# Optimization experiments

Hardware: AMD Instinct MI355X
Metric: run time of the kernel (lower is better)

Reference implementation:

```python
import jax, jax.numpy as jnp
import numpy as np

SCALE = 8.0  # sqrt(head_dim=64)

def setup_inputs() -> dict:
    key = jax.random.key(0)
    kq, kk, kv = jax.random.split(key, 3)
    B, H, S, D = 2, 16, 2048, 64
    return {
        "query": jax.random.normal(kq, (B, H, S, D), dtype=jnp.float32),
        "key": jax.random.normal(kk, (B, H, S, D), dtype=jnp.float32),
        "value": jax.random.normal(kv, (B, H, S, D), dtype=jnp.float32),
        "mask": jnp.ones((B, 1, 1, S), dtype=jnp.int32),
    }

def reference(query, key, value, mask):
    # scores: [B,H,S,S]
    scores = jnp.einsum("bhqd,bhkd->bhqk", query, key) / SCALE
    scores = jnp.where(mask == 0, -jnp.inf, scores)
    attn_probs = jax.nn.softmax(scores, axis=-1)
    # dropout_rate = 0.0 -> identity
    output = jnp.einsum("bhqk,bhkd->bhqd", attn_probs, value)
    return (output, attn_probs)
```

## Files before the change

kernel.cpp:

```cpp
#include <hip/hip_runtime.h>

#define B_  2
#define H_  16
#define S_  2048
#define D_  64
#define BH_ (B_*H_)
#define QT  64
#define KT  64
#define NKT (S_/KT)
#define LDQ 72

typedef __attribute__((ext_vector_type(8))) short bf16x8;
typedef __attribute__((ext_vector_type(4))) float f32x4;

static __device__ __forceinline__ ushort f2bf(float f) {
  union { float f; unsigned u; } v; v.f = f;
  unsigned r = (v.u + 0x7fff + ((v.u >> 16) & 1)) >> 16;
  return (ushort)r;
}

static __device__ __forceinline__ void score_tiles(
    f32x4 acc[4], const ushort* __restrict__ sK, const bf16x8 qa[2],
    int l15, int lq, const int* __restrict__ mg, int kbase)
{
#pragma unroll
  for (int t = 0; t < 4; ++t) {
    const bf16x8 kb0 = *(const bf16x8*)&sK[(t*16 + l15)*LDQ +      lq*8];
    const bf16x8 kb1 = *(const bf16x8*)&sK[(t*16 + l15)*LDQ + 32 + lq*8];
    f32x4 a = {0.f, 0.f, 0.f, 0.f};
    a = __builtin_amdgcn_mfma_f32_16x16x32_bf16(qa[0], kb0, a, 0, 0, 0);
    a = __builtin_amdgcn_mfma_f32_16x16x32_bf16(qa[1], kb1, a, 0, 0, 0);
    const int mv = mg[kbase + t*16 + l15];
    if (mv == 0) { a[0] = -1e30f; a[1] = -1e30f; a[2] = -1e30f; a[3] = -1e30f; }
    acc[t] = a;
  }
}

__global__ __launch_bounds__(256)
void attn_kernel(const float* __restrict__ Q, const float* __restrict__ K,
                 const float* __restrict__ V, const int* __restrict__ mask,
                 float* __restrict__ outO, float* __restrict__ outP)
{
  __shared__ ushort sQ[QT * LDQ];
  __shared__ ushort sK[KT * LDQ];
  __shared__ ushort sVt[D_ * LDQ];
  __shared__ ushort sP[4][16 * LDQ];

  const int tid  = threadIdx.x;
  const int wave = tid >> 6;
  const int lane = tid & 63;
  const int l15  = lane & 15;
  const int lq   = lane >> 4;

  const int qt = blockIdx.x;
  const int bh = blockIdx.y;
  const int b  = bh >> 4;
  const int q0 = qt * QT;

  const float* Qg = Q + (size_t)(bh*S_ + q0) * D_;
  const float* Kg = K + (size_t)bh * S_ * D_;
  const float* Vg = V + (size_t)bh * S_ * D_;
  const int*   mg = mask + b * S_;
  float* Og = outO + (size_t)(bh*S_ + q0) * D_;
  float* Pg = outP + ((size_t)(bh*S_ + q0)) * S_;

  const int srow = tid >> 2;
  const int sd0  = (tid & 3) * 16;

  {
    const float* src = Qg + (size_t)srow * D_ + sd0;
    ushort* dst = &sQ[srow*LDQ + sd0];
#pragma unroll
    for (int i = 0; i < 16; i += 4) {
      float4 v = *(const float4*)(src + i);
      dst[i+0] = f2bf(v.x * 0.125f);
      dst[i+1] = f2bf(v.y * 0.125f);
      dst[i+2] = f2bf(v.z * 0.125f);
      dst[i+3] = f2bf(v.w * 0.125f);
    }
  }
  __syncthreads();

  bf16x8 qa[2];
#pragma unroll
  for (int c = 0; c < 2; ++c)
    qa[c] = *(const bf16x8*)&sQ[(wave*16 + l15)*LDQ + c*32 + lq*8];

  float m_r[4] = {-1e30f, -1e30f, -1e30f, -1e30f};
  float l_r[4] = {0.f, 0.f, 0.f, 0.f};

  for (int kt = 0; kt < NKT; ++kt) {
    __syncthreads();
    {
      const float* src = Kg + (size_t)(kt*KT + srow) * D_ + sd0;
      ushort* dst = &sK[srow*LDQ + sd0];
#pragma unroll
      for (int i = 0; i < 16; i += 4) {
        float4 v = *(const float4*)(src + i);
        dst[i+0] = f2bf(v.x); dst[i+1] = f2bf(v.y);
        dst[i+2] = f2bf(v.z); dst[i+3] = f2bf(v.w);
      }
    }
    __syncthreads();

    f32x4 acc[4];
    score_tiles(acc, sK, qa, l15, lq, mg, kt*KT);

#pragma unroll
    for (int j = 0; j < 4; ++j) {
      float v = fmaxf(fmaxf(acc[0][j], acc[1][j]), fmaxf(acc[2][j], acc[3][j]));
#pragma unroll
      for (int s = 1; s < 16; s <<= 1) v = fmaxf(v, __shfl_xor(v, s));
      const float mn = fmaxf(m_r[j], v);
      float ps = __expf(acc[0][j] - mn) + __expf(acc[1][j] - mn)
               + __expf(acc[2][j] - mn) + __expf(acc[3][j] - mn);
#pragma unroll
      for (int s = 1; s < 16; s <<= 1) ps += __shfl_xor(ps, s);
      l_r[j] = l_r[j] * __expf(m_r[j] - mn) + ps;
      m_r[j] = mn;
    }
  }

  float inv_l[4];
#pragma unroll
  for (int j = 0; j < 4; ++j) inv_l[j] = 1.0f / l_r[j];

  f32x4 oacc[4];
#pragma unroll
  for (int n = 0; n < 4; ++n) { oacc[n][0]=0.f; oacc[n][1]=0.f; oacc[n][2]=0.f; oacc[n][3]=0.f; }

  ushort* sPw = &sP[wave][0];

  for (int kt = 0; kt < NKT; ++kt) {
    __syncthreads();
    {
      const float* src = Kg + (size_t)(kt*KT + srow) * D_ + sd0;
      ushort* dst = &sK[srow*LDQ + sd0];
#pragma unroll
      for (int i = 0; i < 16; i += 4) {
        float4 v = *(const float4*)(src + i);
        dst[i+0] = f2bf(v.x); dst[i+1] = f2bf(v.y);
        dst[i+2] = f2bf(v.z); dst[i+3] = f2bf(v.w);
      }
    }
    {
      const int vkey = tid & 63;
      const int vd0  = (tid >> 6) * 16;
      const float* vsrc = Vg + (size_t)(kt*KT + vkey) * D_ + vd0;
#pragma unroll
      for (int i = 0; i < 16; i += 4) {
        float4 v = *(const float4*)(vsrc + i);
        sVt[(vd0+i+0)*LDQ + vkey] = f2bf(v.x);
        sVt[(vd0+i+1)*LDQ + vkey] = f2bf(v.y);
        sVt[(vd0+i+2)*LDQ + vkey] = f2bf(v.z);
        sVt[(vd0+i+3)*LDQ + vkey] = f2bf(v.w);
      }
    }
    __syncthreads();

    f32x4 acc[4];
    score_tiles(acc, sK, qa, l15, lq, mg, kt*KT);

#pragma unroll
    for (int t = 0; t < 4; ++t) {
#pragma unroll
      for (int j = 0; j < 4; ++j) {
        const float p = __expf(acc[t][j] - m_r[j]) * inv_l[j];
        sPw[(lq*4 + j)*LDQ + t*16 + l15] = f2bf(p);
      }
    }
    __syncthreads();

#pragma unroll
    for (int i = 0; i < 4; ++i) {
      const int r = lq + i*4;
      const ushort* ps = &sPw[r*LDQ + l15*4];
      float4 o;
      o.x = __uint_as_float((unsigned)ps[0] << 16);
      o.y = __uint_as_float((unsigned)ps[1] << 16);
      o.z = __uint_as_float((unsigned)ps[2] << 16);
      o.w = __uint_as_float((unsigned)ps[3] << 16);
      *(float4*)&Pg[(size_t)(wave*16 + r)*S_ + kt*KT + l15*4] = o;
    }

#pragma unroll
    for (int c = 0; c < 2; ++c) {
      const bf16x8 pa = *(const bf16x8*)&sPw[l15*LDQ + c*32 + lq*8];
#pragma unroll
      for (int n = 0; n < 4; ++n) {
        const bf16x8 vb = *(const bf16x8*)&sVt[(n*16 + l15)*LDQ + c*32 + lq*8];
        oacc[n] = __builtin_amdgcn_mfma_f32_16x16x32_bf16(pa, vb, oacc[n], 0, 0, 0);
      }
    }
  }

#pragma unroll
  for (int n = 0; n < 4; ++n) {
#pragma unroll
    for (int j = 0; j < 4; ++j) {
      Og[(size_t)(wave*16 + lq*4 + j)*D_ + n*16 + l15] = oacc[n][j];
    }
  }
}

extern "C" void kernel_launch(void* const* d_in, const int* in_sizes, int n_in,
                              void* d_out, int out_size, void* d_ws, size_t ws_size,
                              hipStream_t stream) {
  const float* Q = (const float*)d_in[0];
  const float* K = (const float*)d_in[1];
  const float* V = (const float*)d_in[2];
  const int* mask = (const int*)d_in[3];
  float* outO = (float*)d_out;
  float* outP = outO + (size_t)B_ * H_ * S_ * D_;
  dim3 grid(S_ / QT, BH_);
  attn_kernel<<<grid, dim3(256), 0, stream>>>(Q, K, V, mask, outO, outP);
}
```

Before: 776.5 us.

## Pre-convert Q/K/V to swizzled bf16 tiles and double-buffer async LDS loads

Adds a conversion kernel that turns Q (scaled by log2e/8), K, and transposed V into bf16 64x64 tiles with an XOR swizzle, stored in the workspace. The main kernel then stages these tiles into double-buffered LDS with global_load_lds, prefetching the next tile while computing on the current one. The softmax switches to exp2 with a single logsumexp offset, and the cross-lane max/sum reduction moves out of the first pass to the end. This removes the repeated fp32 loads and conversions of K/V in every query block, at the cost of an extra launch and workspace traffic. The old kernel is kept as a fallback when the workspace is too small.

```diff
diff --git a/kernel.cpp b/kernel.cpp
--- a/kernel.cpp
+++ b/kernel.cpp
@@ -5,13 +5,16 @@
 #define S_  2048
 #define D_  64
 #define BH_ (B_*H_)
-#define QT  64
-#define KT  64
-#define NKT (S_/KT)
+#define NKT (S_/64)
 #define LDQ 72
+#define LDP 72
 
 typedef __attribute__((ext_vector_type(8))) short bf16x8;
 typedef __attribute__((ext_vector_type(4))) float f32x4;
+typedef __attribute__((address_space(1))) const char gchar;
+typedef __attribute__((address_space(3))) char lchar;
+
+#define QK_SCALE 0.18033688011112042f
 
 static __device__ __forceinline__ ushort f2bf(float f) {
   union { float f; unsigned u; } v; v.f = f;
@@ -19,7 +22,228 @@
   return (ushort)r;
 }
 
-static __device__ __forceinline__ void score_tiles(
+static __device__ __forceinline__ uint4 pack8(const float* e, float sc) {
+  uint4 p;
+  p.x = (unsigned)f2bf(e[0]*sc) | ((unsigned)f2bf(e[1]*sc) << 16);
+  p.y = (unsigned)f2bf(e[2]*sc) | ((unsigned)f2bf(e[3]*sc) << 16);
+  p.z = (unsigned)f2bf(e[4]*sc) | ((unsigned)f2bf(e[5]*sc) << 16);
+  p.w = (unsigned)f2bf(e[6]*sc) | ((unsigned)f2bf(e[7]*sc) << 16);
+  return p;
+}
+
+__global__ __launch_bounds__(256)
+void conv_kernel(const float* __restrict__ Q, const float* __restrict__ K,
+                 const float* __restrict__ V,
+                 ushort* __restrict__ Qw, ushort* __restrict__ Kw, ushort* __restrict__ Vw)
+{
+  const int tile = blockIdx.x, bh = blockIdx.y, mode = blockIdx.z;
+  const int tid = threadIdx.x;
+  const float* src = (mode == 0 ? Q : (mode == 1 ? K : V)) + ((size_t)bh*S_ + tile*64) * D_;
+  ushort* dst = (mode == 0 ? Qw : (mode == 1 ? Kw : Vw)) + ((size_t)bh*NKT + tile) * 4096;
+
+  const int r  = tid >> 2;
+  const int c0 = (tid & 3) * 16;
+
+  if (mode < 2) {
+    const float sc = (mode == 0) ? QK_SCALE : 1.0f;
+    const float4* s4 = (const float4*)(src + (size_t)r*D_ + c0);
+    float e[16];
+#pragma unroll
+    for (int i = 0; i < 4; ++i) {
+      float4 v = s4[i];
+      e[i*4+0] = v.x; e[i*4+1] = v.y; e[i*4+2] = v.z; e[i*4+3] = v.w;
+    }
+#pragma unroll
+    for (int g = 0; g < 2; ++g) {
+      const int gi = ((c0 >> 3) + g) ^ (r & 7);
+      *(uint4*)((char*)dst + r*128 + gi*16) = pack8(e + g*8, sc);
+    }
+  } else {
+    __shared__ float t[64][65];
+    const float4* s4 = (const float4*)(src + (size_t)r*D_ + c0);
+#pragma unroll
+    for (int i = 0; i < 4; ++i) {
+      float4 v = s4[i];
+      t[r][c0 + i*4 + 0] = v.x; t[r][c0 + i*4 + 1] = v.y;
+      t[r][c0 + i*4 + 2] = v.z; t[r][c0 + i*4 + 3] = v.w;
+    }
+    __syncthreads();
+    float e[16];
+#pragma unroll
+    for (int i = 0; i < 16; ++i) e[i] = t[c0 + i][r];
+#pragma unroll
+    for (int g = 0; g < 2; ++g) {
+      const int gi = ((c0 >> 3) + g) ^ (r & 7);
+      *(uint4*)((char*)dst + r*128 + gi*16) = pack8(e + g*8, 1.0f);
+    }
+  }
+}
+
+static __device__ __forceinline__ void stage8k(void* lds, const void* src, int wave, int lane) {
+  const char* s = (const char*)src + lane*16;
+  char* d = (char*)lds;
+#pragma unroll
+  for (int i = 0; i < 2; ++i) {
+    const int off = (wave + i*4) << 10;
+    __builtin_amdgcn_global_load_lds((gchar*)(s + off), (lchar*)(d + off), 16, 0, 0);
+  }
+}
+
+__global__ __launch_bounds__(256, 3)
+void attn2_kernel(const ushort* __restrict__ Qw, const ushort* __restrict__ Kw,
+                  const ushort* __restrict__ Vw, const int* __restrict__ mask,
+                  float* __restrict__ outO, float* __restrict__ outP)
+{
+  __shared__ ushort sQ[4096];
+  __shared__ ushort sK[2][4096];
+  __shared__ ushort sVt[2][4096];
+  __shared__ ushort sP[4][16 * LDP];
+
+  const int tid  = threadIdx.x;
+  const int wave = tid >> 6;
+  const int lane = tid & 63;
+  const int l15  = lane & 15;
+  const int lq   = lane >> 4;
+  const int rxor = l15 & 7;
+
+  const int qt = blockIdx.x;
+  const int bh = blockIdx.y;
+  const int b  = bh >> 4;
+
+  const ushort* Qt = Qw + ((size_t)bh*NKT + qt) * 4096;
+  const ushort* Kt = Kw + (size_t)bh*NKT * 4096;
+  const ushort* Vt = Vw + (size_t)bh*NKT * 4096;
+  const int*    mg = mask + b * S_;
+  float* Og = outO + (size_t)(bh*S_ + qt*64) * D_;
+  float* Pg = outP + (size_t)(bh*S_ + qt*64) * S_;
+
+  stage8k(sQ, Qt, wave, lane);
+  stage8k(sK[0], Kt, wave, lane);
+  __syncthreads();
+
+  bf16x8 qa[2];
+#pragma unroll
+  for (int c = 0; c < 2; ++c)
+    qa[c] = *(const bf16x8*)((const char*)sQ + (wave*16 + l15)*128 + (((c*4 + lq) ^ rxor) << 4));
+
+  float m_r[4] = {-1e30f, -1e30f, -1e30f, -1e30f};
+  float l_r[4] = {0.f, 0.f, 0.f, 0.f};
+
+  int cur = 0;
+  for (int kt = 0; kt < NKT; ++kt) {
+    if (kt + 1 < NKT) stage8k(sK[cur ^ 1], Kt + (size_t)(kt + 1)*4096, wave, lane);
+    int mv[4];
+#pragma unroll
+    for (int t = 0; t < 4; ++t) mv[t] = mg[kt*64 + t*16 + l15];
+    f32x4 acc[4];
+#pragma unroll
+    for (int t = 0; t < 4; ++t) {
+      const char* rowp = (const char*)sK[cur] + (t*16 + l15)*128;
+      const bf16x8 kb0 = *(const bf16x8*)(rowp + (((0 + lq) ^ rxor) << 4));
+      const bf16x8 kb1 = *(const bf16x8*)(rowp + (((4 + lq) ^ rxor) << 4));
+      f32x4 a = {0.f, 0.f, 0.f, 0.f};
+      a = __builtin_amdgcn_mfma_f32_16x16x32_bf16(qa[0], kb0, a, 0, 0, 0);
+      a = __builtin_amdgcn_mfma_f32_16x16x32_bf16(qa[1], kb1, a, 0, 0, 0);
+      if (mv[t] == 0) { a[0] = -1e30f; a[1] = -1e30f; a[2] = -1e30f; a[3] = -1e30f; }
+      acc[t] = a;
+    }
+#pragma unroll
+    for (int j = 0; j < 4; ++j) {
+      const float vmax = fmaxf(fmaxf(acc[0][j], acc[1][j]), fmaxf(acc[2][j], acc[3][j]));
+      const float mn = fmaxf(m_r[j], vmax);
+      const float ps = __builtin_amdgcn_exp2f(acc[0][j] - mn) + __builtin_amdgcn_exp2f(acc[1][j] - mn)
+                     + __builtin_amdgcn_exp2f(acc[2][j] - mn) + __builtin_amdgcn_exp2f(acc[3][j] - mn);
+      l_r[j] = l_r[j] * __builtin_amdgcn_exp2f(m_r[j] - mn) + ps;
+      m_r[j] = mn;
+    }
+    __syncthreads();
+    cur ^= 1;
+  }
+
+  float madj[4];
+#pragma unroll
+  for (int j = 0; j < 4; ++j) {
+    float m = m_r[j], l = l_r[j];
+#pragma unroll
+    for (int s = 1; s < 16; s <<= 1) {
+      const float om = __shfl_xor(m, s);
+      const float ol = __shfl_xor(l, s);
+      const float mn = fmaxf(m, om);
+      l = l * __builtin_amdgcn_exp2f(m - mn) + ol * __builtin_amdgcn_exp2f(om - mn);
+      m = mn;
+    }
+    madj[j] = m + __builtin_amdgcn_logf(l);
+  }
+
+  f32x4 oacc[4];
+#pragma unroll
+  for (int n = 0; n < 4; ++n) { oacc[n][0]=0.f; oacc[n][1]=0.f; oacc[n][2]=0.f; oacc[n][3]=0.f; }
+  ushort* sPw = &sP[wave][0];
+
+  stage8k(sK[0], Kt, wave, lane);
+  stage8k(sVt[0], Vt, wave, lane);
+  cur = 0;
+  __syncthreads();
+
+  for (int kt = 0; kt < NKT; ++kt) {
+    if (kt + 1 < NKT) {
+      stage8k(sK[cur ^ 1], Kt + (size_t)(kt + 1)*4096, wave, lane);
+      stage8k(sVt[cur ^ 1], Vt + (size_t)(kt + 1)*4096, wave, lane);
+    }
+    int mv[4];
+#pragma unroll
+    for (int t = 0; t < 4; ++t) mv[t] = mg[kt*64 + t*16 + l15];
+    f32x4 acc[4];
+#pragma unroll
+    for (int t = 0; t < 4; ++t) {
+      const char* rowp = (const char*)sK[cur] + (t*16 + l15)*128;
+      const bf16x8 kb0 = *(const bf16x8*)(rowp + (((0 + lq) ^ rxor) << 4));
+      const bf16x8 kb1 = *(const bf16x8*)(rowp + (((4 + lq) ^ rxor) << 4));
+      f32x4 a = {0.f, 0.f, 0.f, 0.f};
+      a = __builtin_amdgcn_mfma_f32_16x16x32_bf16(qa[0], kb0, a, 0, 0, 0);
+      a = __builtin_amdgcn_mfma_f32_16x16x32_bf16(qa[1], kb1, a, 0, 0, 0);
+      if (mv[t] == 0) { a[0] = -1e30f; a[1] = -1e30f; a[2] = -1e30f; a[3] = -1e30f; }
+      acc[t] = a;
+    }
+#pragma unroll
+    for (int t = 0; t < 4; ++t) {
+#pragma unroll
+      for (int j = 0; j < 4; ++j) {
+        sPw[(lq*4 + j)*LDP + t*16 + l15] = f2bf(__builtin_amdgcn_exp2f(acc[t][j] - madj[j]));
+      }
+    }
+#pragma unroll
+    for (int i = 0; i < 4; ++i) {
+      const int r = lq + i*4;
+      const ushort* ps = &sPw[r*LDP + l15*4];
+      float4 o;
+      o.x = __uint_as_float((unsigned)ps[0] << 16);
+      o.y = __uint_as_float((unsigned)ps[1] << 16);
+      o.z = __uint_as_float((unsigned)ps[2] << 16);
+      o.w = __uint_as_float((unsigned)ps[3] << 16);
+      *(float4*)&Pg[(size_t)(wave*16 + r)*S_ + kt*64 + l15*4] = o;
+    }
+#pragma unroll
+    for (int c2 = 0; c2 < 2; ++c2) {
+      const bf16x8 pa = *(const bf16x8*)((const char*)sPw + l15*(LDP*2) + c2*64 + lq*16);
+#pragma unroll
+      for (int n = 0; n < 4; ++n) {
+        const bf16x8 vb = *(const bf16x8*)((const char*)sVt[cur] + (n*16 + l15)*128 + (((c2*4 + lq) ^ rxor) << 4));
+        oacc[n] = __builtin_amdgcn_mfma_f32_16x16x32_bf16(pa, vb, oacc[n], 0, 0, 0);
+      }
+    }
+    __syncthreads();
+    cur ^= 1;
+  }
+
+#pragma unroll
+  for (int n = 0; n < 4; ++n)
+#pragma unroll
+    for (int j = 0; j < 4; ++j)
+      Og[(size_t)(wave*16 + lq*4 + j)*D_ + n*16 + l15] = oacc[n][j];
+}
+
+static __device__ __forceinline__ void score_tiles_fb(
     f32x4 acc[4], const ushort* __restrict__ sK, const bf16x8 qa[2],
     int l15, int lq, const int* __restrict__ mg, int kbase)
 {
@@ -41,8 +265,8 @@
                  const float* __restrict__ V, const int* __restrict__ mask,
                  float* __restrict__ outO, float* __restrict__ outP)
 {
-  __shared__ ushort sQ[QT * LDQ];
-  __shared__ ushort sK[KT * LDQ];
+  __shared__ ushort sQ[64 * LDQ];
+  __shared__ ushort sK[64 * LDQ];
   __shared__ ushort sVt[D_ * LDQ];
   __shared__ ushort sP[4][16 * LDQ];
 
@@ -51,11 +275,10 @@
   const int lane = tid & 63;
   const int l15  = lane & 15;
   const int lq   = lane >> 4;
-
   const int qt = blockIdx.x;
   const int bh = blockIdx.y;
   const int b  = bh >> 4;
-  const int q0 = qt * QT;
+  const int q0 = qt * 64;
 
   const float* Qg = Q + (size_t)(bh*S_ + q0) * D_;
   const float* Kg = K + (size_t)bh * S_ * D_;
@@ -73,10 +296,8 @@
 #pragma unroll
     for (int i = 0; i < 16; i += 4) {
       float4 v = *(const float4*)(src + i);
-      dst[i+0] = f2bf(v.x * 0.125f);
-      dst[i+1] = f2bf(v.y * 0.125f);
-      dst[i+2] = f2bf(v.z * 0.125f);
-      dst[i+3] = f2bf(v.w * 0.125f);
+      dst[i+0] = f2bf(v.x * 0.125f); dst[i+1] = f2bf(v.y * 0.125f);
+      dst[i+2] = f2bf(v.z * 0.125f); dst[i+3] = f2bf(v.w * 0.125f);
     }
   }
   __syncthreads();
@@ -92,7 +313,7 @@
   for (int kt = 0; kt < NKT; ++kt) {
     __syncthreads();
     {
-      const float* src = Kg + (size_t)(kt*KT + srow) * D_ + sd0;
+      const float* src = Kg + (size_t)(kt*64 + srow) * D_ + sd0;
       ushort* dst = &sK[srow*LDQ + sd0];
 #pragma unroll
       for (int i = 0; i < 16; i += 4) {
@@ -102,10 +323,8 @@
       }
     }
     __syncthreads();
-
     f32x4 acc[4];
-    score_tiles(acc, sK, qa, l15, lq, mg, kt*KT);
-
+    score_tiles_fb(acc, sK, qa, l15, lq, mg, kt*64);
 #pragma unroll
     for (int j = 0; j < 4; ++j) {
       float v = fmaxf(fmaxf(acc[0][j], acc[1][j]), fmaxf(acc[2][j], acc[3][j]));
@@ -128,13 +347,12 @@
   f32x4 oacc[4];
 #pragma unroll
   for (int n = 0; n < 4; ++n) { oacc[n][0]=0.f; oacc[n][1]=0.f; oacc[n][2]=0.f; oacc[n][3]=0.f; }
-
   ushort* sPw = &sP[wave][0];
 
   for (int kt = 0; kt < NKT; ++kt) {
     __syncthreads();
     {
-      const float* src = Kg + (size_t)(kt*KT + srow) * D_ + sd0;
+      const float* src = Kg + (size_t)(kt*64 + srow) * D_ + sd0;
       ushort* dst = &sK[srow*LDQ + sd0];
 #pragma unroll
       for (int i = 0; i < 16; i += 4) {
@@ -146,7 +364,7 @@
     {
       const int vkey = tid & 63;
       const int vd0  = (tid >> 6) * 16;
-      const float* vsrc = Vg + (size_t)(kt*KT + vkey) * D_ + vd0;
+      const float* vsrc = Vg + (size_t)(kt*64 + vkey) * D_ + vd0;
 #pragma unroll
       for (int i = 0; i < 16; i += 4) {
         float4 v = *(const float4*)(vsrc + i);
@@ -157,20 +375,16 @@
       }
     }
     __syncthreads();
-
     f32x4 acc[4];
-    score_tiles(acc, sK, qa, l15, lq, mg, kt*KT);
-
-#pragma unroll
-    for (int t = 0; t < 4; ++t) {
+    score_tiles_fb(acc, sK, qa, l15, lq, mg, kt*64);
+#pragma unroll
+    for (int t = 0; t < 4; ++t)
 #pragma unroll
       for (int j = 0; j < 4; ++j) {
         const float p = __expf(acc[t][j] - m_r[j]) * inv_l[j];
         sPw[(lq*4 + j)*LDQ + t*16 + l15] = f2bf(p);
       }
-    }
-    __syncthreads();
-
+    __syncthreads();
 #pragma unroll
     for (int i = 0; i < 4; ++i) {
       const int r = lq + i*4;
@@ -180,9 +394,8 @@
       o.y = __uint_as_float((unsigned)ps[1] << 16);
       o.z = __uint_as_float((unsigned)ps[2] << 16);
       o.w = __uint_as_float((unsigned)ps[3] << 16);
-      *(float4*)&Pg[(size_t)(wave*16 + r)*S_ + kt*KT + l15*4] = o;
-    }
-
+      *(float4*)&Pg[(size_t)(wave*16 + r)*S_ + kt*64 + l15*4] = o;
+    }
 #pragma unroll
     for (int c = 0; c < 2; ++c) {
       const bf16x8 pa = *(const bf16x8*)&sPw[l15*LDQ + c*32 + lq*8];
@@ -193,14 +406,11 @@
       }
     }
   }
-
-#pragma unroll
-  for (int n = 0; n < 4; ++n) {
-#pragma unroll
-    for (int j = 0; j < 4; ++j) {
+#pragma unroll
+  for (int n = 0; n < 4; ++n)
+#pragma unroll
+    for (int j = 0; j < 4; ++j)
       Og[(size_t)(wave*16 + lq*4 + j)*D_ + n*16 + l15] = oacc[n][j];
-    }
-  }
 }
 
 extern "C" void kernel_launch(void* const* d_in, const int* in_sizes, int n_in,
@@ -212,6 +422,15 @@
   const int* mask = (const int*)d_in[3];
   float* outO = (float*)d_out;
   float* outP = outO + (size_t)B_ * H_ * S_ * D_;
-  dim3 grid(S_ / QT, BH_);
-  attn_kernel<<<grid, dim3(256), 0, stream>>>(Q, K, V, mask, outO, outP);
-}
+
+  const size_t elems = (size_t)B_ * H_ * S_ * D_;
+  if (ws_size >= elems * 2 * 3) {
+    ushort* Qw = (ushort*)d_ws;
+    ushort* Kw = Qw + elems;
+    ushort* Vw = Kw + elems;
+    conv_kernel<<<dim3(NKT, BH_, 3), dim3(256), 0, stream>>>(Q, K, V, Qw, Kw, Vw);
+    attn2_kernel<<<dim3(S_/64, BH_), dim3(256), 0, stream>>>(Qw, Kw, Vw, mask, outO, outP);
+  } else {
+    attn_kernel<<<dim3(S_/64, BH_), dim3(256), 0, stream>>>(Q, K, V, mask, outO, outP);
+  }
+}
```

After: 707.2 us. -8.9%, faster.
